# Optimization experiments

Measured on AMD Instinct MI355X. Metric: run time of the kernel, lower is better.

## Reference

```python
import jax, jax.numpy as jnp
import numpy as np

EPS = 1e-6

def _rmsnorm(x, w):
    # normalize over last (head_dim) axis
    return x * jax.lax.rsqrt(jnp.mean(x * x, axis=-1, keepdims=True) + EPS) * w

def _rope(x, cos, sin):
    # x: [B, H, S, D]; cos/sin: [S, D]
    d = x.shape[-1]
    x1, x2 = x[..., : d // 2], x[..., d // 2 :]
    rot = jnp.concatenate([-x2, x1], axis=-1)
    return x * cos[None, None] + rot * sin[None, None]

def setup_inputs() -> dict:
    key = jax.random.key(0)
    B, S, D_MODEL = 1, 2048, 2048
    HEADS, HEAD_DIM, NKV = 32, 64, 8
    d_out = HEADS * HEAD_DIM
    kv_d_out = NKV * HEAD_DIM
    ks = jax.random.split(key, 8)
    x = jax.random.normal(ks[0], (B, S, D_MODEL), dtype=jnp.float32)
    # RoPE tables
    inv_freq = 1.0 / (10000.0 ** (jnp.arange(0, HEAD_DIM, 2, dtype=jnp.float32) / HEAD_DIM))
    pos = jnp.arange(S, dtype=jnp.float32)
    ang = pos[:, None] * inv_freq[None, :]            # [S, D/2]
    ang = jnp.concatenate([ang, ang], axis=-1)        # [S, D]
    sin, cos = jnp.sin(ang), jnp.cos(ang)
    mask = jnp.tril(jnp.ones((S, S), dtype=bool))     # causal: True = attend
    sd = 0.02
    Wq = jax.random.normal(ks[1], (D_MODEL, d_out), dtype=jnp.float32) * sd
    Wk = jax.random.normal(ks[2], (D_MODEL, kv_d_out), dtype=jnp.float32) * sd
    Wv = jax.random.normal(ks[3], (D_MODEL, kv_d_out), dtype=jnp.float32) * sd
    Wo = jax.random.normal(ks[4], (d_out, D_MODEL), dtype=jnp.float32) * sd
    bo = jnp.zeros((D_MODEL,), dtype=jnp.float32)
    q_scale = jnp.ones((HEAD_DIM,), dtype=jnp.float32)
    k_scale = jnp.ones((HEAD_DIM,), dtype=jnp.float32)
    return {"x": x, "sin": sin, "cos": cos, "mask": mask, "Wq": Wq, "Wk": Wk,
            "Wv": Wv, "Wo": Wo, "bo": bo, "q_scale": q_scale, "k_scale": k_scale}

def reference(x, sin, cos, mask, Wq, Wk, Wv, Wo, bo, q_scale, k_scale):
    B, S, _ = x.shape
    HEADS, HEAD_DIM, NKV = 32, 64, 8
    GS = HEADS // NKV  # group size = 4
    q = (x @ Wq).reshape(B, S, HEADS, HEAD_DIM).transpose(0, 2, 1, 3)  # [B,H,S,D]
    k = (x @ Wk).reshape(B, S, NKV, HEAD_DIM).transpose(0, 2, 1, 3)    # [B,G,S,D]
    v = (x @ Wv).reshape(B, S, NKV, HEAD_DIM).transpose(0, 2, 1, 3)    # [B,G,S,D]
    q = _rmsnorm(q, q_scale)
    k = _rmsnorm(k, k_scale)
    q = _rope(q, cos, sin)
    k = _rope(k, cos, sin)
    # GQA without materializing repeated k/v: group query heads per kv group
    qg = q.reshape(B, NKV, GS, S, HEAD_DIM)
    scale = 1.0 / jnp.sqrt(jnp.asarray(HEAD_DIM, dtype=x.dtype))
    scores = jnp.einsum('bghqd,bgkd->bghqk', qg, k) * scale  # [B,G,Gs,S,S]
    scores = jnp.where(mask[None, None, None], scores, jnp.asarray(-jnp.inf, dtype=scores.dtype))
    attn = jax.nn.softmax(scores, axis=-1)
    out = jnp.einsum('bghqk,bgkd->bghqd', attn, v)            # [B,G,Gs,S,D]
    out = out.reshape(B, HEADS, S, HEAD_DIM).transpose(0, 2, 1, 3).reshape(B, S, HEADS * HEAD_DIM)
    return out @ Wo + bo
```

## Files before the change

### kernel.cpp

```cpp
#include <hip/hip_runtime.h>
#include <stdint.h>


typedef __bf16 bf16x8 __attribute__((ext_vector_type(8)));
typedef __bf16 bf16x4v __attribute__((ext_vector_type(4)));
typedef float f32x4 __attribute__((ext_vector_type(4)));

#define MFMA_BF16(a, b, c) __builtin_amdgcn_mfma_f32_16x16x32_bf16(a, b, c, 0, 0, 0)

#if __has_builtin(__builtin_amdgcn_exp2f)
#define EXP2F(x) __builtin_amdgcn_exp2f(x)
#else
#define EXP2F(x) __expf((x) * 0.69314718055994531f)
#endif

#define QSCALE 0.18033688011112042f
#define SHIFT2 11.541560327111707f

__device__ __forceinline__ unsigned short f2bf(float f) {
  unsigned int u = __float_as_uint(f);
  u += 0x7fffu + ((u >> 16) & 1u);
  return (unsigned short)(u >> 16);
}
__device__ __forceinline__ float bf2f(unsigned short b) {
  return __uint_as_float(((unsigned int)b) << 16);
}

__device__ __forceinline__ void gload_lds16(const unsigned short* gsrc,
                                            unsigned short* ldst) {
  __builtin_amdgcn_global_load_lds(
      (const __attribute__((address_space(1))) unsigned int*)gsrc,
      (__attribute__((address_space(3))) unsigned int*)ldst, 16, 0, 0);
}

__global__ __launch_bounds__(256) void cvt_bf16(const float* __restrict__ X,
                                                unsigned short* __restrict__ Y, int n) {
  int i = (blockIdx.x * 256 + threadIdx.x) * 4;
  if (i < n) {
    float4 v = *(const float4*)&X[i];
    ushort4 o;
    o.x = f2bf(v.x); o.y = f2bf(v.y); o.z = f2bf(v.z); o.w = f2bf(v.w);
    *(ushort4*)&Y[i] = o;
  }
}

__global__ __launch_bounds__(256) void transpose_all(const float* __restrict__ Wq,
                                                     const float* __restrict__ Wk,
                                                     const float* __restrict__ Wv,
                                                     const float* __restrict__ Wo,
                                                     unsigned short* __restrict__ Wqkvt,
                                                     unsigned short* __restrict__ Wot) {
  int bx = blockIdx.x;
  const float* W;
  unsigned short* T;
  int N, nb;
  if (bx < 32)      { W = Wq; T = Wqkvt;                       N = 2048; nb = bx * 64; }
  else if (bx < 40) { W = Wk; T = Wqkvt + 2048 * 2048;         N = 512;  nb = (bx - 32) * 64; }
  else if (bx < 48) { W = Wv; T = Wqkvt + (size_t)2560 * 2048; N = 512;  nb = (bx - 40) * 64; }
  else              { W = Wo; T = Wot;                         N = 2048; nb = (bx - 48) * 64; }
  int kb = blockIdx.y * 64;
  int tid = threadIdx.x;
  __shared__ float tile[64][65];
#pragma unroll
  for (int i = 0; i < 16; i++) {
    int idx = tid + i * 256;
    int r = idx >> 6, c = idx & 63;
    tile[r][c] = W[(size_t)(kb + r) * N + nb + c];
  }
  __syncthreads();
#pragma unroll
  for (int i = 0; i < 8; i++) {
    int idx = tid + i * 256;
    int r = idx >> 5, cp = idx & 31;
    ushort2 o;
    o.x = f2bf(tile[2 * cp][r]);
    o.y = f2bf(tile[2 * cp + 1][r]);
    *(ushort2*)&T[(size_t)(nb + r) * 2048 + kb + 2 * cp] = o;
  }
}

#define GEMM_DBUF(A_, B_, m0_, n0_)                                            \
  int quad = lane >> 4, l16 = lane & 15;                                       \
  int wrow = (w & 1) * 32, wcol = (w >> 1) * 64;                               \
  int rsub = lane >> 3, csub = lane & 7;                                       \
  int chunk = csub ^ rsub;                                                     \
  int slotL = quad ^ (l16 & 7);                                                \
  const unsigned short* gA = &A_[(size_t)(m0_ + w * 16 + rsub) * 2048 + chunk * 8]; \
  const unsigned short* gB = &B_[(size_t)(n0_ + w * 32 + rsub) * 2048 + chunk * 8]; \
  int laOff = (w * 16) * 64 + lane * 8;                                        \
  int lbOff = 64 * 64 + (w * 32) * 64 + lane * 8;                              \
  f32x4 acc[2][4];                                                             \
  _Pragma("unroll") for (int i = 0; i < 2; i++)                                \
      _Pragma("unroll") for (int j = 0; j < 4; j++)                            \
          acc[i][j] = (f32x4){0.f, 0.f, 0.f, 0.f};                             \
  {                                                                            \
    unsigned short* sp = &Stage[0][0];                                         \
    gload_lds16(gA, sp + laOff);                                               \
    gload_lds16(gA + 8 * 2048, sp + laOff + 8 * 64);                           \
    gload_lds16(gB, sp + lbOff);                                               \
    gload_lds16(gB + 8 * 2048, sp + lbOff + 8 * 64);                           \
    gload_lds16(gB + 16 * 2048, sp + lbOff + 16 * 64);                         \
    gload_lds16(gB + 24 * 2048, sp + lbOff + 24 * 64);                         \
  }                                                                            \
  for (int k0 = 0; k0 < 2048; k0 += 64) {                                      \
    __syncthreads();                                                           \
    unsigned short* cur = &Stage[(k0 >> 6) & 1][0];                            \
    unsigned short* nxt = &Stage[((k0 >> 6) + 1) & 1][0];                      \
    if (k0 + 64 < 2048) {                                                      \
      int kn = k0 + 64;                                                        \
      gload_lds16(gA + kn, nxt + laOff);                                       \
      gload_lds16(gA + 8 * 2048 + kn, nxt + laOff + 8 * 64);                   \
      gload_lds16(gB + kn, nxt + lbOff);                                       \
      gload_lds16(gB + 8 * 2048 + kn, nxt + lbOff + 8 * 64);                   \
      gload_lds16(gB + 16 * 2048 + kn, nxt + lbOff + 16 * 64);                 \
      gload_lds16(gB + 24 * 2048 + kn, nxt + lbOff + 24 * 64);                 \
    }                                                                          \
    const unsigned short* As = cur;                                            \
    const unsigned short* Bs = cur + 64 * 64;                                  \
    bf16x8 af[2][2], bfr[4][2];                                                \
    _Pragma("unroll") for (int i = 0; i < 2; i++) {                            \
      int base = (wrow + i * 16 + l16) * 64;                                   \
      af[i][0] = *(const bf16x8*)&As[base + slotL * 8];                        \
      af[i][1] = *(const bf16x8*)&As[base + (slotL ^ 4) * 8];                  \
    }                                                                          \
    _Pragma("unroll") for (int j = 0; j < 4; j++) {                            \
      int base = (wcol + j * 16 + l16) * 64;                                   \
      bfr[j][0] = *(const bf16x8*)&Bs[base + slotL * 8];                       \
      bfr[j][1] = *(const bf16x8*)&Bs[base + (slotL ^ 4) * 8];                 \
    }                                                                          \
    _Pragma("unroll") for (int kc = 0; kc < 2; kc++)                           \
        _Pragma("unroll") for (int i = 0; i < 2; i++)                          \
            _Pragma("unroll") for (int j = 0; j < 4; j++)                      \
                acc[i][j] = MFMA_BF16(af[i][kc], bfr[j][kc], acc[i][j]);       \
  }

__global__ __launch_bounds__(256, 3) void gemm_qkv(const unsigned short* __restrict__ A,
                                                   const unsigned short* __restrict__ B,
                                                   const float* __restrict__ sinp,
                                                   const float* __restrict__ cosp,
                                                   const float* __restrict__ q_scale,
                                                   const float* __restrict__ k_scale,
                                                   unsigned short* __restrict__ qh,
                                                   unsigned short* __restrict__ kh,
                                                   unsigned short* __restrict__ vtmp) {
  __shared__ __align__(16) unsigned short Stage[2][192 * 64];
  int tid = threadIdx.x;
  int w = tid >> 6, lane = tid & 63;
  int m0 = blockIdx.y * 64;
  int n0 = blockIdx.x * 128;
  GEMM_DBUF(A, B, m0, n0)

  int hd = blockIdx.x * 2 + (w >> 1);
  if (hd < 40) {
    const float* scl = (hd < 32) ? q_scale : k_scale;
    float wsc[4];
#pragma unroll
    for (int j = 0; j < 4; j++) wsc[j] = scl[j * 16 + l16];
    float oscale = (hd < 32) ? QSCALE : 1.0f;
#pragma unroll
    for (int i = 0; i < 2; i++)
#pragma unroll
      for (int r = 0; r < 4; r++) {
        float ss = 0.f;
#pragma unroll
        for (int j = 0; j < 4; j++) ss += acc[i][j][r] * acc[i][j][r];
#pragma unroll
        for (int off = 8; off; off >>= 1) ss += __shfl_xor(ss, off);
        float inv = rsqrtf(ss * (1.f / 64.f) + 1e-6f);
        int s = m0 + wrow + i * 16 + quad * 4 + r;
        float xn[4];
#pragma unroll
        for (int j = 0; j < 4; j++) xn[j] = acc[i][j][r] * inv * wsc[j];
#pragma unroll
        for (int j = 0; j < 4; j++) {
          int d = j * 16 + l16;
          float rot = (j < 2) ? -xn[j + 2] : xn[j - 2];
          float out = (xn[j] * cosp[s * 64 + d] + rot * sinp[s * 64 + d]) * oscale;
          if (hd < 32) qh[(size_t)s * 2048 + hd * 64 + d] = f2bf(out);
          else         kh[(size_t)s * 512 + (hd - 32) * 64 + d] = f2bf(out);
        }
      }
  } else {
    int g = hd - 40;
#pragma unroll
    for (int i = 0; i < 2; i++)
#pragma unroll
      for (int r = 0; r < 4; r++) {
        int s = m0 + wrow + i * 16 + quad * 4 + r;
#pragma unroll
        for (int j = 0; j < 4; j++)
          vtmp[(size_t)s * 512 + g * 64 + j * 16 + l16] = f2bf(acc[i][j][r]);
      }
  }
}

__global__ __launch_bounds__(256, 3) void gemm_out(const unsigned short* __restrict__ A,
                                                   const unsigned short* __restrict__ B,
                                                   float* __restrict__ C,
                                                   const float* __restrict__ bias) {
  __shared__ __align__(16) unsigned short Stage[2][192 * 64];
  int tid = threadIdx.x;
  int w = tid >> 6, lane = tid & 63;
  int m0 = blockIdx.y * 64;
  int n0 = blockIdx.x * 128;
  GEMM_DBUF(A, B, m0, n0)

#pragma unroll
  for (int i = 0; i < 2; i++) {
    int row = m0 + wrow + i * 16 + quad * 4;
#pragma unroll
    for (int j = 0; j < 4; j++) {
      int col = n0 + wcol + j * 16 + l16;
      float b = bias[col];
#pragma unroll
      for (int r = 0; r < 4; r++)
        C[(size_t)(row + r) * 2048 + col] = acc[i][j][r] + b;
    }
  }
}

__global__ __launch_bounds__(256) void v_transpose(const unsigned short* __restrict__ vtmp,
                                                   unsigned short* __restrict__ vt) {
  __shared__ unsigned short tile[64][65];
  int s0 = blockIdx.x * 64;
  int g = blockIdx.y;
  int tid = threadIdx.x;
#pragma unroll
  for (int i = 0; i < 16; i++) {
    int idx = tid + i * 256;
    int r = idx >> 6, c = idx & 63;
    tile[r][c] = vtmp[(size_t)(s0 + r) * 512 + g * 64 + c];
  }
  __syncthreads();
#pragma unroll
  for (int i = 0; i < 16; i++) {
    int idx = tid + i * 256;
    int d = idx >> 6, slot = idx & 63;
    int key = (slot & 3) * 16 + (slot >> 2);
    vt[(size_t)(g * 64 + d) * 2048 + s0 + slot] = tile[key][d];
  }
}

__global__ __launch_bounds__(256, 4) void attention(const unsigned short* __restrict__ qh,
                                                    const unsigned short* __restrict__ kh,
                                                    const unsigned short* __restrict__ vt,
                                                    unsigned short* __restrict__ Opart,
                                                    float* __restrict__ Lpart) {
  int h = blockIdx.y;
  int g = h >> 2;
  int z = blockIdx.z;
  int tile = (blockIdx.x + blockIdx.y) & 31;
  int q0 = tile * 64;
  int w = threadIdx.x >> 6;
  int lane = threadIdx.x & 63;
  int quad = lane >> 4;
  int l16 = lane & 15;
  int qrow0 = q0 + w * 16;

  __shared__ __align__(16) unsigned short Stage[2][8192];
  __shared__ __align__(16) unsigned short Plds[4][16 * 72];
  unsigned short* P = &Plds[w][0];

  int rsub = lane >> 3;
  int csub = lane & 7;
  int chunk = csub ^ rsub;

  const unsigned short* kg = &kh[(size_t)(w * 16 + rsub) * 512 + g * 64 + chunk * 8];
  const unsigned short* vg = &vt[(size_t)(g * 64 + w * 16 + rsub) * 2048 + chunk * 8];
  int klOff = (w * 16) * 64 + lane * 8;
  int vlOff = 4096 + (w * 16) * 64 + lane * 8;

  int posL = quad ^ (l16 & 7);
  int fL = l16 * 64 + posL * 8;
  int fH = l16 * 64 + (posL ^ 4) * 8;

  bf16x8 aq0 = *(const bf16x8*)&qh[(size_t)(qrow0 + l16) * 2048 + h * 64 + quad * 8];
  bf16x8 aq1 = *(const bf16x8*)&qh[(size_t)(qrow0 + l16) * 2048 + h * 64 + 32 + quad * 8];

  f32x4 o[4];
#pragma unroll
  for (int j = 0; j < 4; j++) o[j] = (f32x4){0.f, 0.f, 0.f, 0.f};
  float l_run[4] = {0.f, 0.f, 0.f, 0.f};

  int T = tile + 1;
  int it0 = z ? (T >> 1) : 0;
  int it1 = z ? T : (T >> 1);
  if (it0 < it1) {
    unsigned short* sp = &Stage[0][0];
    int n0 = it0 << 6;
    gload_lds16(kg + (size_t)n0 * 512, sp + klOff);
    gload_lds16(kg + (size_t)(n0 + 8) * 512, sp + klOff + 8 * 64);
    gload_lds16(vg + n0, sp + vlOff);
    gload_lds16(vg + n0 + 8 * 2048, sp + vlOff + 8 * 64);
  }
  for (int it = it0; it < it1; ++it) {
    __syncthreads();
    const unsigned short* cur = &Stage[(it - it0) & 1][0];
    unsigned short* nxt = &Stage[(it - it0 + 1) & 1][0];
    if (it + 1 < it1) {
      int nn = (it + 1) << 6;
      gload_lds16(kg + (size_t)nn * 512, nxt + klOff);
      gload_lds16(kg + (size_t)(nn + 8) * 512, nxt + klOff + 8 * 64);
      gload_lds16(vg + nn, nxt + vlOff);
      gload_lds16(vg + nn + 8 * 2048, nxt + vlOff + 8 * 64);
    }
    int n0 = it << 6;
    const unsigned short* Ks = cur;
    const unsigned short* Vs = cur + 4096;

    f32x4 s[4];
#pragma unroll
    for (int t = 0; t < 4; ++t) {
      bf16x8 kfl = *(const bf16x8*)&Ks[t * 1024 + fL];
      bf16x8 kfh = *(const bf16x8*)&Ks[t * 1024 + fH];
      f32x4 zz = (f32x4){0.f, 0.f, 0.f, 0.f};
      zz = MFMA_BF16(aq0, kfl, zz);
      s[t] = MFMA_BF16(aq1, kfh, zz);
    }

    float pv[4][4];
    if (it == T - 1) {
#pragma unroll
      for (int t = 0; t < 4; ++t) {
        int key = n0 + t * 16 + l16;
#pragma unroll
        for (int r = 0; r < 4; ++r) {
          int row = qrow0 + quad * 4 + r;
          float p = (key <= row) ? EXP2F(s[t][r] - SHIFT2) : 0.f;
          l_run[r] += p;
          pv[t][r] = p;
        }
      }
    } else {
#pragma unroll
      for (int t = 0; t < 4; ++t)
#pragma unroll
        for (int r = 0; r < 4; ++r) {
          float p = EXP2F(s[t][r] - SHIFT2);
          l_run[r] += p;
          pv[t][r] = p;
        }
    }
#pragma unroll
    for (int r = 0; r < 4; ++r) {
      bf16x4v pk;
      pk[0] = (__bf16)pv[0][r]; pk[1] = (__bf16)pv[1][r];
      pk[2] = (__bf16)pv[2][r]; pk[3] = (__bf16)pv[3][r];
      *(bf16x4v*)&P[(quad * 4 + r) * 72 + l16 * 4] = pk;
    }
    __threadfence_block();
    bf16x8 pf0 = *(const bf16x8*)&P[l16 * 72 + quad * 8];
    bf16x8 pf1 = *(const bf16x8*)&P[l16 * 72 + 32 + quad * 8];

#pragma unroll
    for (int j = 0; j < 4; ++j) {
      bf16x8 vfl = *(const bf16x8*)&Vs[j * 1024 + fL];
      bf16x8 vfh = *(const bf16x8*)&Vs[j * 1024 + fH];
      o[j] = MFMA_BF16(pf0, vfl, o[j]);
      o[j] = MFMA_BF16(pf1, vfh, o[j]);
    }
  }

#pragma unroll
  for (int r = 0; r < 4; r++) {
    float sum = l_run[r];
#pragma unroll
    for (int off = 8; off; off >>= 1) sum += __shfl_xor(sum, off);
    if (l16 == 0)
      Lpart[(size_t)z * 65536 + (qrow0 + quad * 4 + r) * 32 + h] = sum;
  }
#pragma unroll
  for (int j = 0; j < 4; j++)
#pragma unroll
    for (int r = 0; r < 4; r++)
      Opart[((size_t)z * 2048 + qrow0 + quad * 4 + r) * 2048 + h * 64 + j * 16 + l16] =
          f2bf(o[j][r]);
}

__global__ __launch_bounds__(256) void combine(const unsigned short* __restrict__ Opart,
                                               const float* __restrict__ Lpart,
                                               unsigned short* __restrict__ aout) {
  int idx = blockIdx.x * 256 + threadIdx.x;
  int s = idx >> 9;
  int col = (idx & 511) * 4;
  int h = col >> 6;
  float l = Lpart[s * 32 + h] + Lpart[65536 + s * 32 + h];
  float linv = 1.f / l;
  ushort4 a = *(const ushort4*)&Opart[(size_t)s * 2048 + col];
  ushort4 b = *(const ushort4*)&Opart[(size_t)(2048 + s) * 2048 + col];
  ushort4 o;
  o.x = f2bf((bf2f(a.x) + bf2f(b.x)) * linv);
  o.y = f2bf((bf2f(a.y) + bf2f(b.y)) * linv);
  o.z = f2bf((bf2f(a.z) + bf2f(b.z)) * linv);
  o.w = f2bf((bf2f(a.w) + bf2f(b.w)) * linv);
  *(ushort4*)&aout[(size_t)s * 2048 + col] = o;
}

extern "C" void kernel_launch(void* const* d_in, const int* in_sizes, int n_in,
                              void* d_out, int out_size, void* d_ws, size_t ws_size,
                              hipStream_t stream) {
  (void)in_sizes; (void)n_in; (void)out_size; (void)ws_size;
  const float* x    = (const float*)d_in[0];
  const float* sinp = (const float*)d_in[1];
  const float* cosp = (const float*)d_in[2];
  const float* Wq = (const float*)d_in[4];
  const float* Wk = (const float*)d_in[5];
  const float* Wv = (const float*)d_in[6];
  const float* Wo = (const float*)d_in[7];
  const float* bo = (const float*)d_in[8];
  const float* q_scale = (const float*)d_in[9];
  const float* k_scale = (const float*)d_in[10];
  float* outp = (float*)d_out;

  uint8_t* ws = (uint8_t*)d_ws;
  const size_t MB = 1024 * 1024;
  unsigned short* xb    = (unsigned short*)(ws);
  unsigned short* Wqkvt = (unsigned short*)(ws + 8 * MB);
  unsigned short* Wot   = (unsigned short*)(ws + 20 * MB);
  unsigned short* qh    = (unsigned short*)(ws + 28 * MB);
  unsigned short* kh    = (unsigned short*)(ws + 36 * MB);
  unsigned short* vtmp  = (unsigned short*)(ws + 38 * MB);
  unsigned short* vt    = (unsigned short*)(ws + 40 * MB);
  unsigned short* aout  = (unsigned short*)(ws + 42 * MB);
  unsigned short* Opart = (unsigned short*)(ws + 50 * MB);
  float*          Lpart = (float*)(ws + 66 * MB);

  cvt_bf16<<<4096, 256, 0, stream>>>(x, xb, 2048 * 2048);
  transpose_all<<<dim3(80, 32), 256, 0, stream>>>(Wq, Wk, Wv, Wo, Wqkvt, Wot);
  gemm_qkv<<<dim3(24, 32), 256, 0, stream>>>(xb, Wqkvt, sinp, cosp, q_scale, k_scale,
                                             qh, kh, vtmp);
  v_transpose<<<dim3(32, 8), 256, 0, stream>>>(vtmp, vt);
  attention<<<dim3(32, 32, 2), 256, 0, stream>>>(qh, kh, vt, Opart, Lpart);
  combine<<<4096, 256, 0, stream>>>(Opart, Lpart, aout);
  gemm_out<<<dim3(16, 32), 256, 0, stream>>>(aout, Wot, outp, bo);
}
```

Measured before the change: 236.3 us.

## Share K/V tiles across all four GQA heads per attention block

Measured after the change: 233.7 us. No clear change (-1.1%).

```diff
diff --git a/kernel.cpp b/kernel.cpp
--- a/kernel.cpp
+++ b/kernel.cpp
@@ -241,24 +241,23 @@
   }
 }
 
-__global__ __launch_bounds__(256, 4) void attention(const unsigned short* __restrict__ qh,
+__global__ __launch_bounds__(256, 2) void attention(const unsigned short* __restrict__ qh,
                                                     const unsigned short* __restrict__ kh,
                                                     const unsigned short* __restrict__ vt,
                                                     unsigned short* __restrict__ Opart,
                                                     float* __restrict__ Lpart) {
-  int h = blockIdx.y;
-  int g = h >> 2;
+  int g = blockIdx.y;
   int z = blockIdx.z;
-  int tile = (blockIdx.x + blockIdx.y) & 31;
+  int tile = (blockIdx.x + blockIdx.y * 4) & 31;
   int q0 = tile * 64;
   int w = threadIdx.x >> 6;
+  int h = g * 4 + w;
   int lane = threadIdx.x & 63;
   int quad = lane >> 4;
   int l16 = lane & 15;
-  int qrow0 = q0 + w * 16;
 
   __shared__ __align__(16) unsigned short Stage[2][8192];
-  __shared__ __align__(16) unsigned short Plds[4][16 * 72];
+  __shared__ __align__(16) unsigned short Plds[4][64 * 72];
   unsigned short* P = &Plds[w][0];
 
   int rsub = lane >> 3;
@@ -274,13 +273,24 @@
   int fL = l16 * 64 + posL * 8;
   int fH = l16 * 64 + (posL ^ 4) * 8;
 
-  bf16x8 aq0 = *(const bf16x8*)&qh[(size_t)(qrow0 + l16) * 2048 + h * 64 + quad * 8];
-  bf16x8 aq1 = *(const bf16x8*)&qh[(size_t)(qrow0 + l16) * 2048 + h * 64 + 32 + quad * 8];
-
-  f32x4 o[4];
-#pragma unroll
-  for (int j = 0; j < 4; j++) o[j] = (f32x4){0.f, 0.f, 0.f, 0.f};
-  float l_run[4] = {0.f, 0.f, 0.f, 0.f};
+  bf16x8 aq[4][2];
+#pragma unroll
+  for (int i = 0; i < 4; i++) {
+    const unsigned short* qp = &qh[(size_t)(q0 + i * 16 + l16) * 2048 + h * 64 + quad * 8];
+    aq[i][0] = *(const bf16x8*)qp;
+    aq[i][1] = *(const bf16x8*)(qp + 32);
+  }
+
+  f32x4 o[4][4];
+#pragma unroll
+  for (int i = 0; i < 4; i++)
+#pragma unroll
+    for (int j = 0; j < 4; j++) o[i][j] = (f32x4){0.f, 0.f, 0.f, 0.f};
+  float l_run[4][4];
+#pragma unroll
+  for (int i = 0; i < 4; i++)
+#pragma unroll
+    for (int r = 0; r < 4; r++) l_run[i][r] = 0.f;
 
   int T = tile + 1;
   int it0 = z ? (T >> 1) : 0;
@@ -307,74 +317,93 @@
     int n0 = it << 6;
     const unsigned short* Ks = cur;
     const unsigned short* Vs = cur + 4096;
-
-    f32x4 s[4];
+    bool diag = (it == T - 1);
+
+    bf16x8 kf[4][2];
 #pragma unroll
     for (int t = 0; t < 4; ++t) {
-      bf16x8 kfl = *(const bf16x8*)&Ks[t * 1024 + fL];
-      bf16x8 kfh = *(const bf16x8*)&Ks[t * 1024 + fH];
-      f32x4 zz = (f32x4){0.f, 0.f, 0.f, 0.f};
-      zz = MFMA_BF16(aq0, kfl, zz);
-      s[t] = MFMA_BF16(aq1, kfh, zz);
-    }
-
-    float pv[4][4];
-    if (it == T - 1) {
+      kf[t][0] = *(const bf16x8*)&Ks[t * 1024 + fL];
+      kf[t][1] = *(const bf16x8*)&Ks[t * 1024 + fH];
+    }
+
+#pragma unroll
+    for (int i = 0; i < 4; ++i) {
+      f32x4 s[4];
 #pragma unroll
       for (int t = 0; t < 4; ++t) {
-        int key = n0 + t * 16 + l16;
-#pragma unroll
-        for (int r = 0; r < 4; ++r) {
-          int row = qrow0 + quad * 4 + r;
-          float p = (key <= row) ? EXP2F(s[t][r] - SHIFT2) : 0.f;
-          l_run[r] += p;
-          pv[t][r] = p;
+        f32x4 zz = (f32x4){0.f, 0.f, 0.f, 0.f};
+        zz = MFMA_BF16(aq[i][0], kf[t][0], zz);
+        s[t] = MFMA_BF16(aq[i][1], kf[t][1], zz);
+      }
+      float pv[4][4];
+      if (diag) {
+#pragma unroll
+        for (int t = 0; t < 4; ++t) {
+          int key = n0 + t * 16 + l16;
+#pragma unroll
+          for (int r = 0; r < 4; ++r) {
+            int row = q0 + i * 16 + quad * 4 + r;
+            float p = (key <= row) ? EXP2F(s[t][r] - SHIFT2) : 0.f;
+            l_run[i][r] += p;
+            pv[t][r] = p;
+          }
         }
-      }
-    } else {
-#pragma unroll
-      for (int t = 0; t < 4; ++t)
-#pragma unroll
-        for (int r = 0; r < 4; ++r) {
-          float p = EXP2F(s[t][r] - SHIFT2);
-          l_run[r] += p;
-          pv[t][r] = p;
-        }
-    }
-#pragma unroll
-    for (int r = 0; r < 4; ++r) {
-      bf16x4v pk;
-      pk[0] = (__bf16)pv[0][r]; pk[1] = (__bf16)pv[1][r];
-      pk[2] = (__bf16)pv[2][r]; pk[3] = (__bf16)pv[3][r];
-      *(bf16x4v*)&P[(quad * 4 + r) * 72 + l16 * 4] = pk;
+      } else {
+#pragma unroll
+        for (int t = 0; t < 4; ++t)
+#pragma unroll
+          for (int r = 0; r < 4; ++r) {
+            float p = EXP2F(s[t][r] - SHIFT2);
+            l_run[i][r] += p;
+            pv[t][r] = p;
+          }
+      }
+#pragma unroll
+      for (int r = 0; r < 4; ++r) {
+        bf16x4v pk;
+        pk[0] = (__bf16)pv[0][r]; pk[1] = (__bf16)pv[1][r];
+        pk[2] = (__bf16)pv[2][r]; pk[3] = (__bf16)pv[3][r];
+        *(bf16x4v*)&P[(i * 16 + quad * 4 + r) * 72 + l16 * 4] = pk;
+      }
     }
     __threadfence_block();
-    bf16x8 pf0 = *(const bf16x8*)&P[l16 * 72 + quad * 8];
-    bf16x8 pf1 = *(const bf16x8*)&P[l16 * 72 + 32 + quad * 8];
-
+
+    bf16x8 vf[4][2];
 #pragma unroll
     for (int j = 0; j < 4; ++j) {
-      bf16x8 vfl = *(const bf16x8*)&Vs[j * 1024 + fL];
-      bf16x8 vfh = *(const bf16x8*)&Vs[j * 1024 + fH];
-      o[j] = MFMA_BF16(pf0, vfl, o[j]);
-      o[j] = MFMA_BF16(pf1, vfh, o[j]);
-    }
-  }
-
-#pragma unroll
-  for (int r = 0; r < 4; r++) {
-    float sum = l_run[r];
-#pragma unroll
-    for (int off = 8; off; off >>= 1) sum += __shfl_xor(sum, off);
-    if (l16 == 0)
-      Lpart[(size_t)z * 65536 + (qrow0 + quad * 4 + r) * 32 + h] = sum;
-  }
-#pragma unroll
-  for (int j = 0; j < 4; j++)
-#pragma unroll
-    for (int r = 0; r < 4; r++)
-      Opart[((size_t)z * 2048 + qrow0 + quad * 4 + r) * 2048 + h * 64 + j * 16 + l16] =
-          f2bf(o[j][r]);
+      vf[j][0] = *(const bf16x8*)&Vs[j * 1024 + fL];
+      vf[j][1] = *(const bf16x8*)&Vs[j * 1024 + fH];
+    }
+#pragma unroll
+    for (int i = 0; i < 4; ++i) {
+      bf16x8 pf0 = *(const bf16x8*)&P[(i * 16 + l16) * 72 + quad * 8];
+      bf16x8 pf1 = *(const bf16x8*)&P[(i * 16 + l16) * 72 + 32 + quad * 8];
+#pragma unroll
+      for (int j = 0; j < 4; ++j) {
+        o[i][j] = MFMA_BF16(pf0, vf[j][0], o[i][j]);
+        o[i][j] = MFMA_BF16(pf1, vf[j][1], o[i][j]);
+      }
+    }
+  }
+
+#pragma unroll
+  for (int i = 0; i < 4; i++)
+#pragma unroll
+    for (int r = 0; r < 4; r++) {
+      float sum = l_run[i][r];
+#pragma unroll
+      for (int off = 8; off; off >>= 1) sum += __shfl_xor(sum, off);
+      if (l16 == 0)
+        Lpart[(size_t)z * 65536 + (q0 + i * 16 + quad * 4 + r) * 32 + h] = sum;
+    }
+#pragma unroll
+  for (int i = 0; i < 4; i++)
+#pragma unroll
+    for (int j = 0; j < 4; j++)
+#pragma unroll
+      for (int r = 0; r < 4; r++)
+        Opart[((size_t)z * 2048 + q0 + i * 16 + quad * 4 + r) * 2048 + h * 64 + j * 16 + l16] =
+            f2bf(o[i][j][r]);
 }
 
 __global__ __launch_bounds__(256) void combine(const unsigned short* __restrict__ Opart,
@@ -430,7 +459,7 @@
   gemm_qkv<<<dim3(24, 32), 256, 0, stream>>>(xb, Wqkvt, sinp, cosp, q_scale, k_scale,
                                              qh, kh, vtmp);
   v_transpose<<<dim3(32, 8), 256, 0, stream>>>(vtmp, vt);
-  attention<<<dim3(32, 32, 2), 256, 0, stream>>>(qh, kh, vt, Opart, Lpart);
+  attention<<<dim3(32, 8, 2), 256, 0, stream>>>(qh, kh, vt, Opart, Lpart);
   combine<<<4096, 256, 0, stream>>>(Opart, Lpart, aout);
   gemm_out<<<dim3(16, 32), 256, 0, stream>>>(aout, Wot, outp, bo);
 }
```

## Transpose attention MFMAs so P stays in registers, drop LDS P round-trip

Applied to the files above, without the earlier changes.

Result: faster. 222.9 us (-5.6%).

```diff
diff --git a/kernel.cpp b/kernel.cpp
--- a/kernel.cpp
+++ b/kernel.cpp
@@ -236,7 +236,8 @@
   for (int i = 0; i < 16; i++) {
     int idx = tid + i * 256;
     int d = idx >> 6, slot = idx & 63;
-    int key = (slot & 3) * 16 + (slot >> 2);
+    int qd = (slot >> 3) & 3, c = slot >> 5, j = slot & 7;
+    int key = 16 * ((j >> 2) * 2 + c) + qd * 4 + (j & 3);
     vt[(size_t)(g * 64 + d) * 2048 + s0 + slot] = tile[key][d];
   }
 }
@@ -257,9 +258,9 @@
   int l16 = lane & 15;
   int qrow0 = q0 + w * 16;
 
-  __shared__ __align__(16) unsigned short Stage[2][8192];
-  __shared__ __align__(16) unsigned short Plds[4][16 * 72];
-  unsigned short* P = &Plds[w][0];
+  __shared__ __align__(16) unsigned short Stage[8192];
+  unsigned short* Ks = Stage;
+  unsigned short* Vs = Stage + 4096;
 
   int rsub = lane >> 3;
   int csub = lane & 7;
@@ -267,46 +268,32 @@
 
   const unsigned short* kg = &kh[(size_t)(w * 16 + rsub) * 512 + g * 64 + chunk * 8];
   const unsigned short* vg = &vt[(size_t)(g * 64 + w * 16 + rsub) * 2048 + chunk * 8];
-  int klOff = (w * 16) * 64 + lane * 8;
-  int vlOff = 4096 + (w * 16) * 64 + lane * 8;
+  unsigned short* kl = Ks + (w * 16) * 64 + lane * 8;
+  unsigned short* vl = Vs + (w * 16) * 64 + lane * 8;
 
   int posL = quad ^ (l16 & 7);
   int fL = l16 * 64 + posL * 8;
   int fH = l16 * 64 + (posL ^ 4) * 8;
 
-  bf16x8 aq0 = *(const bf16x8*)&qh[(size_t)(qrow0 + l16) * 2048 + h * 64 + quad * 8];
-  bf16x8 aq1 = *(const bf16x8*)&qh[(size_t)(qrow0 + l16) * 2048 + h * 64 + 32 + quad * 8];
+  bf16x8 bq0 = *(const bf16x8*)&qh[(size_t)(qrow0 + l16) * 2048 + h * 64 + quad * 8];
+  bf16x8 bq1 = *(const bf16x8*)&qh[(size_t)(qrow0 + l16) * 2048 + h * 64 + 32 + quad * 8];
 
   f32x4 o[4];
 #pragma unroll
   for (int j = 0; j < 4; j++) o[j] = (f32x4){0.f, 0.f, 0.f, 0.f};
-  float l_run[4] = {0.f, 0.f, 0.f, 0.f};
+  float l_run = 0.f;
 
   int T = tile + 1;
   int it0 = z ? (T >> 1) : 0;
   int it1 = z ? T : (T >> 1);
-  if (it0 < it1) {
-    unsigned short* sp = &Stage[0][0];
-    int n0 = it0 << 6;
-    gload_lds16(kg + (size_t)n0 * 512, sp + klOff);
-    gload_lds16(kg + (size_t)(n0 + 8) * 512, sp + klOff + 8 * 64);
-    gload_lds16(vg + n0, sp + vlOff);
-    gload_lds16(vg + n0 + 8 * 2048, sp + vlOff + 8 * 64);
-  }
   for (int it = it0; it < it1; ++it) {
+    int n0 = it << 6;
     __syncthreads();
-    const unsigned short* cur = &Stage[(it - it0) & 1][0];
-    unsigned short* nxt = &Stage[(it - it0 + 1) & 1][0];
-    if (it + 1 < it1) {
-      int nn = (it + 1) << 6;
-      gload_lds16(kg + (size_t)nn * 512, nxt + klOff);
-      gload_lds16(kg + (size_t)(nn + 8) * 512, nxt + klOff + 8 * 64);
-      gload_lds16(vg + nn, nxt + vlOff);
-      gload_lds16(vg + nn + 8 * 2048, nxt + vlOff + 8 * 64);
-    }
-    int n0 = it << 6;
-    const unsigned short* Ks = cur;
-    const unsigned short* Vs = cur + 4096;
+    gload_lds16(kg + (size_t)n0 * 512, kl);
+    gload_lds16(kg + (size_t)(n0 + 8) * 512, kl + 8 * 64);
+    gload_lds16(vg + n0, vl);
+    gload_lds16(vg + n0 + 8 * 2048, vl + 8 * 64);
+    __syncthreads();
 
     f32x4 s[4];
 #pragma unroll
@@ -314,67 +301,73 @@
       bf16x8 kfl = *(const bf16x8*)&Ks[t * 1024 + fL];
       bf16x8 kfh = *(const bf16x8*)&Ks[t * 1024 + fH];
       f32x4 zz = (f32x4){0.f, 0.f, 0.f, 0.f};
-      zz = MFMA_BF16(aq0, kfl, zz);
-      s[t] = MFMA_BF16(aq1, kfh, zz);
+      zz = MFMA_BF16(kfl, bq0, zz);
+      s[t] = MFMA_BF16(kfh, bq1, zz);
     }
 
     float pv[4][4];
     if (it == T - 1) {
-#pragma unroll
-      for (int t = 0; t < 4; ++t) {
-        int key = n0 + t * 16 + l16;
+      int qg = qrow0 + l16;
+#pragma unroll
+      for (int t = 0; t < 4; ++t)
 #pragma unroll
         for (int r = 0; r < 4; ++r) {
-          int row = qrow0 + quad * 4 + r;
-          float p = (key <= row) ? EXP2F(s[t][r] - SHIFT2) : 0.f;
-          l_run[r] += p;
+          int key = n0 + t * 16 + quad * 4 + r;
+          float p = (key <= qg) ? EXP2F(s[t][r] - SHIFT2) : 0.f;
+          l_run += p;
           pv[t][r] = p;
         }
-      }
     } else {
 #pragma unroll
       for (int t = 0; t < 4; ++t)
 #pragma unroll
         for (int r = 0; r < 4; ++r) {
           float p = EXP2F(s[t][r] - SHIFT2);
-          l_run[r] += p;
+          l_run += p;
           pv[t][r] = p;
         }
     }
-#pragma unroll
-    for (int r = 0; r < 4; ++r) {
-      bf16x4v pk;
-      pk[0] = (__bf16)pv[0][r]; pk[1] = (__bf16)pv[1][r];
-      pk[2] = (__bf16)pv[2][r]; pk[3] = (__bf16)pv[3][r];
-      *(bf16x4v*)&P[(quad * 4 + r) * 72 + l16 * 4] = pk;
+
+    bf16x8 pf0, pf1;
+#pragma unroll
+    for (int j = 0; j < 4; ++j) {
+      pf0[j] = (__bf16)pv[0][j];
+      pf0[j + 4] = (__bf16)pv[2][j];
+      pf1[j] = (__bf16)pv[1][j];
+      pf1[j + 4] = (__bf16)pv[3][j];
     }
-    __threadfence_block();
-    bf16x8 pf0 = *(const bf16x8*)&P[l16 * 72 + quad * 8];
-    bf16x8 pf1 = *(const bf16x8*)&P[l16 * 72 + 32 + quad * 8];
-
-#pragma unroll
-    for (int j = 0; j < 4; ++j) {
-      bf16x8 vfl = *(const bf16x8*)&Vs[j * 1024 + fL];
-      bf16x8 vfh = *(const bf16x8*)&Vs[j * 1024 + fH];
-      o[j] = MFMA_BF16(pf0, vfl, o[j]);
-      o[j] = MFMA_BF16(pf1, vfh, o[j]);
+
+#pragma unroll
+    for (int jd = 0; jd < 4; ++jd) {
+      bf16x8 vfl = *(const bf16x8*)&Vs[jd * 1024 + fL];
+      bf16x8 vfh = *(const bf16x8*)&Vs[jd * 1024 + fH];
+      o[jd] = MFMA_BF16(vfl, pf0, o[jd]);
+      o[jd] = MFMA_BF16(vfh, pf1, o[jd]);
     }
   }
 
-#pragma unroll
-  for (int r = 0; r < 4; r++) {
-    float sum = l_run[r];
-#pragma unroll
-    for (int off = 8; off; off >>= 1) sum += __shfl_xor(sum, off);
-    if (l16 == 0)
-      Lpart[(size_t)z * 65536 + (qrow0 + quad * 4 + r) * 32 + h] = sum;
-  }
-#pragma unroll
-  for (int j = 0; j < 4; j++)
-#pragma unroll
-    for (int r = 0; r < 4; r++)
-      Opart[((size_t)z * 2048 + qrow0 + quad * 4 + r) * 2048 + h * 64 + j * 16 + l16] =
-          f2bf(o[j][r]);
+  l_run += __shfl_xor(l_run, 16);
+  l_run += __shfl_xor(l_run, 32);
+  if (lane < 16)
+    Lpart[(size_t)z * 65536 + (qrow0 + l16) * 32 + h] = l_run;
+
+  __syncthreads();
+  unsigned short* Ob = Stage + w * (16 * 68);
+#pragma unroll
+  for (int jd = 0; jd < 4; ++jd) {
+    bf16x4v pk;
+#pragma unroll
+    for (int r = 0; r < 4; ++r) pk[r] = (__bf16)o[jd][r];
+    *(bf16x4v*)&Ob[l16 * 68 + jd * 16 + quad * 4] = pk;
+  }
+  __threadfence_block();
+#pragma unroll
+  for (int rr = 0; rr < 2; ++rr) {
+    int cidx = rr * 64 + lane;
+    int row = cidx >> 3, ch = cidx & 7;
+    bf16x8 v = *(const bf16x8*)&Ob[row * 68 + ch * 8];
+    *(bf16x8*)&Opart[((size_t)z * 2048 + qrow0 + row) * 2048 + h * 64 + ch * 8] = v;
+  }
 }
 
 __global__ __launch_bounds__(256) void combine(const unsigned short* __restrict__ Opart,
```
